# Kernel optimization log

Measured on AMD Instinct MI355X. Metric: run time of the kernel, lower is better.

## Reference

```python
import jax, jax.numpy as jnp
import numpy as np

D_MODEL = 256
NHEAD = 8
D_HEAD = D_MODEL // NHEAD
DIM_FF = 1024
B, L = 4, 16384
LN_EPS = 1e-5


def _layernorm(x, g, b):
    mu = jnp.mean(x, axis=-1, keepdims=True)
    var = jnp.mean((x - mu) ** 2, axis=-1, keepdims=True)
    return (x - mu) * jax.lax.rsqrt(var + LN_EPS) * g + b


def _phi(x):
    # elu(x) + 1
    return jnp.where(x > 0, x + 1.0, jnp.exp(x))


def setup_inputs() -> dict:
    key = jax.random.key(0)
    ks = jax.random.split(key, 16)
    s_in = 1.0 / np.sqrt(D_MODEL)
    s_ff = 1.0 / np.sqrt(DIM_FF)
    inp = {
        "x": jax.random.normal(ks[0], (B, L, D_MODEL), dtype=jnp.float32),
        "Wq": jax.random.normal(ks[1], (D_MODEL, D_MODEL), dtype=jnp.float32) * s_in,
        "bq": jnp.zeros((D_MODEL,), jnp.float32),
        "Wk": jax.random.normal(ks[2], (D_MODEL, D_MODEL), dtype=jnp.float32) * s_in,
        "bk": jnp.zeros((D_MODEL,), jnp.float32),
        "Wv": jax.random.normal(ks[3], (D_MODEL, D_MODEL), dtype=jnp.float32) * s_in,
        "bv": jnp.zeros((D_MODEL,), jnp.float32),
        "Wo": jax.random.normal(ks[4], (D_MODEL, D_MODEL), dtype=jnp.float32) * s_in,
        "bo": jnp.zeros((D_MODEL,), jnp.float32),
        "W1": jax.random.normal(ks[5], (D_MODEL, DIM_FF), dtype=jnp.float32) * s_in,
        "b1": jnp.zeros((DIM_FF,), jnp.float32),
        "W2": jax.random.normal(ks[6], (DIM_FF, D_MODEL), dtype=jnp.float32) * s_ff,
        "b2": jnp.zeros((D_MODEL,), jnp.float32),
        "ln1_g": jnp.ones((D_MODEL,), jnp.float32),
        "ln1_b": jnp.zeros((D_MODEL,), jnp.float32),
        "ln2_g": jnp.ones((D_MODEL,), jnp.float32),
        "ln2_b": jnp.zeros((D_MODEL,), jnp.float32),
    }
    return inp


def reference(x, Wq, bq, Wk, bk, Wv, bv, Wo, bo, W1, b1, W2, b2, ln1_g, ln1_b, ln2_g, ln2_b):
    Bq, Lq, _ = x.shape
    q = (x @ Wq + bq).reshape(Bq, Lq, NHEAD, D_HEAD)
    k = (x @ Wk + bk).reshape(Bq, Lq, NHEAD, D_HEAD)
    v = (x @ Wv + bv).reshape(Bq, Lq, NHEAD, D_HEAD)
    q_phi = _phi(q)
    k_phi = _phi(k)
    # kv: [B, H, d, e]
    kv = jnp.einsum("blhd,blhe->bhde", k_phi, v)
    k_sum = k_phi.sum(axis=1)  # [B, H, d]
    z = 1.0 / (jnp.einsum("blhd,bhd->blh", q_phi, k_sum) + 1e-6)
    out = jnp.einsum("blhd,bhde,blh->blhe", q_phi, kv, z)
    out = out.reshape(Bq, Lq, D_MODEL) @ Wo + bo
    x = _layernorm(x + out, ln1_g, ln1_b)
    ff = jax.nn.relu(x @ W1 + b1) @ W2 + b2
    x = _layernorm(x + ff, ln2_g, ln2_b)
    return x
```

## Files before the change

kernel.cpp:

```cpp
#include <hip/hip_runtime.h>
#include <hip/hip_bf16.h>
#include <math.h>

#define NTOK   65536
#define L_SEQ  16384

typedef __bf16 bf16_t;
typedef bf16_t bf16x8 __attribute__((ext_vector_type(8)));
typedef bf16_t bf16x4 __attribute__((ext_vector_type(4)));
typedef float  f32x4  __attribute__((ext_vector_type(4)));

__device__ inline float phi_f(float x) { return x > 0.f ? x + 1.f : __expf(x); }

__device__ inline float quad_sum(float v) {
    v += __shfl_xor(v, 1);
    v += __shfl_xor(v, 2);
    v += __shfl_xor(v, 4);
    v += __shfl_xor(v, 8);
    return v;
}

__device__ inline float ld_any(const void* p, size_t i, int f32) {
    return f32 ? ((const float*)p)[i] : (float)((const bf16_t*)p)[i];
}

__device__ inline void async_copy16(const bf16_t* g, bf16_t* l) {
    __builtin_amdgcn_global_load_lds(
        (const __attribute__((address_space(1))) unsigned int*)g,
        (__attribute__((address_space(3))) unsigned int*)l, 16, 0, 0);
}

__device__ inline void stage_swz(const bf16_t* __restrict__ g, bf16_t* lds,
                                 int tid, int nslot, int ulog2, int rowstride) {
    const int umask = (1 << ulog2) - 1;
    for (int s = tid; s < nslot; s += 256) {
        int n = s >> ulog2, j = s & umask;
        int u = j ^ (n & umask);
        async_copy16(g + (size_t)n * rowstride + u * 8, lds + (size_t)s * 8);
    }
}

__device__ inline bf16x8 rd_swz(const bf16_t* lds, int n, int u, int ulog2) {
    int j = u ^ (n & ((1 << ulog2) - 1));
    return *(const bf16x8*)&lds[(((size_t)n << ulog2) + j) * 8];
}

__device__ inline void stage_w2ff(const bf16_t* __restrict__ W2_t, int ch,
                                  bf16_t* lds, int tid) {
    for (int S = tid; S < 1024; S += 256) {
        int r = S >> 3, phys = S & 7;
        int u = phys ^ (r & 7);
        int n = ((u >> 2) << 7) + r;
        int ks = u & 3;
        async_copy16(W2_t + (size_t)n * 1024 + ch * 32 + ks * 8, lds + (size_t)S * 8);
    }
}

__device__ inline bf16x8 rd_w2ff(const bf16_t* lds, int n, int quad) {
    int r = n & 127;
    int u = ((n >> 7) << 2) + quad;
    int phys = u ^ (r & 7);
    return *(const bf16x8*)&lds[(size_t)(r * 8 + phys) * 8];
}

__device__ inline void hs_put(bf16_t* hs, int r, int c, bf16_t v) {
    int phys = (c >> 3) ^ (r & 15);
    hs[r * 128 + phys * 8 + (c & 7)] = v;
}
__device__ inline bf16x8 hs_get8(const bf16_t* hs, int r, int u) {
    int phys = u ^ (r & 15);
    return *(const bf16x8*)&hs[r * 128 + phys * 8];
}

__device__ inline void ld_afrags(const bf16_t* __restrict__ tile, int row, int q8,
                                 bf16x8 a[8]) {
#pragma unroll
    for (int kk = 0; kk < 8; ++kk)
        a[kk] = *(const bf16x8*)&tile[(size_t)row * 256 + kk * 32 + q8];
}

__global__ __launch_bounds__(256) void k_detect(const void* __restrict__ xraw,
                                                int* __restrict__ flag) {
    __shared__ int bad;
    if (threadIdx.x == 0) bad = 0;
    __syncthreads();
    const bf16_t* xb = (const bf16_t*)xraw;
    int mybad = 0;
#pragma unroll
    for (int j = 0; j < 16; ++j) {
        float v = fabsf((float)xb[threadIdx.x + 256 * j]);
        if (!(v <= 1000.f)) mybad = 1;
    }
    if (mybad) atomicOr(&bad, 1);
    __syncthreads();
    if (threadIdx.x == 0) *flag = bad;
}

__global__ __launch_bounds__(256) void k_convert(const void* __restrict__ xraw,
                                                 const int* __restrict__ flag,
                                                 bf16_t* __restrict__ xbf) {
    const int f = *flag;
    size_t i = ((size_t)blockIdx.x * 256 + threadIdx.x) * 4;
    if (f) {
        f32x4 v = *(const f32x4*)((const float*)xraw + i);
        bf16x4 o;
#pragma unroll
        for (int j = 0; j < 4; ++j) o[j] = (bf16_t)v[j];
        *(bf16x4*)&xbf[i] = o;
    } else {
        *(bf16x4*)&xbf[i] = *(const bf16x4*)((const bf16_t*)xraw + i);
    }
}

__global__ __launch_bounds__(256) void k_prep(
    const void* __restrict__ Wq, const void* __restrict__ Wk,
    const void* __restrict__ Wv, const void* __restrict__ Wo,
    const void* __restrict__ W1, const void* __restrict__ W2,
    const void* __restrict__ bq, const void* __restrict__ bk,
    const void* __restrict__ bv, const void* __restrict__ bo,
    const void* __restrict__ b1, const void* __restrict__ b2,
    const void* __restrict__ g1, const void* __restrict__ be1,
    const void* __restrict__ g2, const void* __restrict__ be2,
    const int* __restrict__ flag,
    bf16_t* __restrict__ Wqkv_t, bf16_t* __restrict__ Wo_t,
    bf16_t* __restrict__ W1_t, bf16_t* __restrict__ W2_t,
    bf16_t* __restrict__ pbuf, float* __restrict__ kvbuf) {
    const int f = *flag;
    int idx = blockIdx.x * 256 + threadIdx.x;
    if (idx < 196608) {
        int n = idx >> 8, k = idx & 255;
        float v;
        if (n < 256)      v = ld_any(Wq, k * 256 + n, f);
        else if (n < 512) v = ld_any(Wk, k * 256 + (n - 256), f);
        else              v = ld_any(Wv, k * 256 + (n - 512), f);
        Wqkv_t[idx] = (bf16_t)v;
    } else if (idx < 262144) {
        int i = idx - 196608; int n = i >> 8, k = i & 255;
        Wo_t[i] = (bf16_t)ld_any(Wo, k * 256 + n, f);
    } else if (idx < 524288) {
        int i = idx - 262144; int n = i >> 8, k = i & 255;
        W1_t[i] = (bf16_t)ld_any(W1, k * 1024 + n, f);
    } else if (idx < 786432) {
        int i = idx - 524288; int n = i >> 10, k = i & 1023;
        W2_t[i] = (bf16_t)ld_any(W2, k * 256 + n, f);
    } else if (idx < 820224) {
        kvbuf[idx - 786432] = 0.f;
    } else if (idx < 823552) {
        int i = idx - 820224;
        float v;
        if (i < 256)        v = ld_any(bq, i, f);
        else if (i < 512)   v = ld_any(bk, i - 256, f);
        else if (i < 768)   v = ld_any(bv, i - 512, f);
        else if (i < 1024)  v = ld_any(bo, i - 768, f);
        else if (i < 2048)  v = ld_any(b1, i - 1024, f);
        else if (i < 2304)  v = ld_any(b2, i - 2048, f);
        else if (i < 2560)  v = ld_any(g1, i - 2304, f);
        else if (i < 2816)  v = ld_any(be1, i - 2560, f);
        else if (i < 3072)  v = ld_any(g2, i - 2816, f);
        else                v = ld_any(be2, i - 3072, f);
        pbuf[i] = (bf16_t)v;
    }
}

__global__ __launch_bounds__(256, 3) void k_qkv(
    const bf16_t* __restrict__ x, const bf16_t* __restrict__ Wqkv_t,
    const bf16_t* __restrict__ pbuf, bf16_t* __restrict__ q_phi) {
    const int mt = blockIdx.x, nt = blockIdx.y;
    const int tid = threadIdx.x, wave = tid >> 6, lane = tid & 63;
    const int l15 = lane & 15, quad = lane >> 4, q8 = quad * 8;
    __shared__ __align__(16) bf16_t bs[128 * 256];
    const int m0 = mt * 128;
    bf16x8 a[2][8];
    ld_afrags(x + (size_t)m0 * 256,        wave * 16 + l15, q8, a[0]);
    ld_afrags(x + (size_t)(m0 + 64) * 256, wave * 16 + l15, q8, a[1]);
    stage_swz(Wqkv_t + (size_t)nt * 128 * 256, bs, tid, 4096, 5, 256);
    __syncthreads();
    f32x4 acc[2][8] = {};
#pragma unroll
    for (int kk = 0; kk < 8; ++kk) {
#pragma unroll
        for (int s = 0; s < 8; ++s) {
            bf16x8 b = rd_swz(bs, s * 16 + l15, kk * 4 + quad, 5);
            acc[0][s] = __builtin_amdgcn_mfma_f32_16x16x32_bf16(a[0][kk], b, acc[0][s], 0, 0, 0);
            acc[1][s] = __builtin_amdgcn_mfma_f32_16x16x32_bf16(a[1][kk], b, acc[1][s], 0, 0, 0);
        }
    }
#pragma unroll
    for (int s = 0; s < 8; ++s) {
        int ng = nt * 128 + s * 16 + l15;
        float bias = (float)pbuf[ng];
#pragma unroll
        for (int mm = 0; mm < 2; ++mm) {
#pragma unroll
            for (int r = 0; r < 4; ++r) {
                int m = m0 + mm * 64 + wave * 16 + quad * 4 + r;
                q_phi[(size_t)m * 256 + ng] = (bf16_t)phi_f(acc[mm][s][r] + bias);
            }
        }
    }
}

__global__ __launch_bounds__(256, 4) void k_kv(
    const bf16_t* __restrict__ x, const bf16_t* __restrict__ Wqkv_t,
    const bf16_t* __restrict__ pbuf, float* __restrict__ kvbuf) {
    const int mt = blockIdx.x, hg = blockIdx.y;
    const int tid = threadIdx.x, wave = tid >> 6, lane = tid & 63;
    const int l15 = lane & 15, quad = lane >> 4, q8 = quad * 8;
    __shared__ __align__(16) bf16_t stg[8192];
    __shared__ __align__(16) bf16_t hsK[4096];
    __shared__ __align__(16) bf16_t hsV[4096];
    const int m0 = mt * 128;
    const int b = m0 >> 14;
    bf16x8 a[2][8];
    ld_afrags(x + (size_t)m0 * 256,        wave * 16 + l15, q8, a[0]);
    ld_afrags(x + (size_t)(m0 + 64) * 256, wave * 16 + l15, q8, a[1]);
    const int td = wave >> 1, te = wave & 1;
    for (int h4 = 0; h4 < 4; ++h4) {
        const int head = hg * 4 + h4;
        const size_t kvbase = (size_t)(b * 8 + head) * 1056;
        stage_swz(Wqkv_t + (size_t)(256 + head * 32) * 256, stg, tid, 1024, 5, 256);
        __syncthreads();
        {
            f32x4 acck[2][2] = {};
#pragma unroll
            for (int kk = 0; kk < 8; ++kk) {
#pragma unroll
                for (int s = 0; s < 2; ++s) {
                    bf16x8 bb = rd_swz(stg, s * 16 + l15, kk * 4 + quad, 5);
                    acck[0][s] = __builtin_amdgcn_mfma_f32_16x16x32_bf16(a[0][kk], bb, acck[0][s], 0, 0, 0);
                    acck[1][s] = __builtin_amdgcn_mfma_f32_16x16x32_bf16(a[1][kk], bb, acck[1][s], 0, 0, 0);
                }
            }
#pragma unroll
            for (int s = 0; s < 2; ++s) {
                float bias = (float)pbuf[256 + head * 32 + s * 16 + l15];
                float kst = 0.f;
#pragma unroll
                for (int mm = 0; mm < 2; ++mm) {
#pragma unroll
                    for (int r = 0; r < 4; ++r) {
                        float v = phi_f(acck[mm][s][r] + bias);
                        kst += v;
                        int c = mm * 64 + wave * 16 + quad * 4 + r;
                        hs_put(hsK, s * 16 + l15, c, (bf16_t)v);
                    }
                }
                kst += __shfl_xor(kst, 16);
                kst += __shfl_xor(kst, 32);
                if (quad == 0)
                    atomicAdd(&kvbuf[kvbase + 1024 + s * 16 + l15], kst);
            }
        }
        __syncthreads();
        stage_swz(Wqkv_t + (size_t)(512 + head * 32) * 256, stg, tid, 1024, 5, 256);
        __syncthreads();
        {
            f32x4 accv[2][2] = {};
#pragma unroll
            for (int kk = 0; kk < 8; ++kk) {
#pragma unroll
                for (int s = 0; s < 2; ++s) {
                    bf16x8 bb = rd_swz(stg, s * 16 + l15, kk * 4 + quad, 5);
                    accv[0][s] = __builtin_amdgcn_mfma_f32_16x16x32_bf16(a[0][kk], bb, accv[0][s], 0, 0, 0);
                    accv[1][s] = __builtin_amdgcn_mfma_f32_16x16x32_bf16(a[1][kk], bb, accv[1][s], 0, 0, 0);
                }
            }
#pragma unroll
            for (int s = 0; s < 2; ++s) {
                float bias = (float)pbuf[512 + head * 32 + s * 16 + l15];
#pragma unroll
                for (int mm = 0; mm < 2; ++mm) {
#pragma unroll
                    for (int r = 0; r < 4; ++r) {
                        int c = mm * 64 + wave * 16 + quad * 4 + r;
                        hs_put(hsV, s * 16 + l15, c, (bf16_t)(accv[mm][s][r] + bias));
                    }
                }
            }
        }
        __syncthreads();
        {
            f32x4 kvacc = {};
#pragma unroll
            for (int kk = 0; kk < 4; ++kk) {
                bf16x8 ak = hs_get8(hsK, td * 16 + l15, kk * 4 + quad);
                bf16x8 bv = hs_get8(hsV, te * 16 + l15, kk * 4 + quad);
                kvacc = __builtin_amdgcn_mfma_f32_16x16x32_bf16(ak, bv, kvacc, 0, 0, 0);
            }
#pragma unroll
            for (int r = 0; r < 4; ++r) {
                int d = td * 16 + quad * 4 + r;
                int e = te * 16 + l15;
                atomicAdd(&kvbuf[kvbase + e * 32 + d], kvacc[r]);
            }
        }
    }
}

__global__ __launch_bounds__(256) void k_kvprep(const float* __restrict__ kvbuf,
                                                bf16_t* __restrict__ kvbf) {
    int idx = blockIdx.x * 256 + threadIdx.x;
    int bh = idx >> 8, r4 = (idx & 255) * 4;
    f32x4 v = *(const f32x4*)&kvbuf[(size_t)bh * 1056 + r4];
    bf16x4 o;
#pragma unroll
    for (int j = 0; j < 4; ++j) o[j] = (bf16_t)v[j];
    *(bf16x4*)&kvbf[(size_t)bh * 1024 + r4] = o;
}

__global__ __launch_bounds__(256, 2) void k_attn_wo_ln1(
    const bf16_t* __restrict__ q_phi, const bf16_t* __restrict__ kvbf,
    const float* __restrict__ kvbuf, const bf16_t* __restrict__ Wo_t,
    const bf16_t* __restrict__ pbuf, const void* __restrict__ xraw,
    const int* __restrict__ flag, bf16_t* __restrict__ x1) {
    const int f = *flag;
    const int mt = blockIdx.x;
    const int tid = threadIdx.x, wave = tid >> 6, lane = tid & 63;
    const int l15 = lane & 15, quad = lane >> 4, q8 = quad * 8;
    __shared__ __align__(16) bf16_t sm0[8192];
    __shared__ __align__(16) bf16_t sm1[16896];
    const int m0 = mt * 128;
    const int b = m0 >> 14;
    stage_swz(Wo_t, sm0, tid, 1024, 5, 256);
    bf16_t* hs = sm1 + wave * (16 * 264);
    const bf16_t* kvb = kvbf + (size_t)b * 8192;
    const float*  ksb = kvbuf + (size_t)b * 8448;
    bf16x8 a2[2][8];
#pragma unroll
    for (int mm = 0; mm < 2; ++mm) {
        bf16x8 a[8];
        ld_afrags(q_phi + (size_t)(m0 + mm * 64) * 256, wave * 16 + l15, q8, a);
#pragma unroll
        for (int h = 0; h < 8; ++h) {
            f32x4 ks0 = *(const f32x4*)&ksb[h * 1056 + 1024 + q8];
            f32x4 ks1 = *(const f32x4*)&ksb[h * 1056 + 1024 + q8 + 4];
            float den = 0.f;
#pragma unroll
            for (int j = 0; j < 4; ++j) den += (float)a[h][j] * ks0[j];
#pragma unroll
            for (int j = 0; j < 4; ++j) den += (float)a[h][4 + j] * ks1[j];
            den += __shfl_xor(den, 16);
            den += __shfl_xor(den, 32);
            float z = 1.f / (den + 1e-6f);
            float zr[4];
#pragma unroll
            for (int r = 0; r < 4; ++r) zr[r] = __shfl(z, quad * 4 + r, 16);
            bf16x8 b0 = *(const bf16x8*)&kvb[h * 1024 + l15 * 32 + q8];
            bf16x8 b1 = *(const bf16x8*)&kvb[h * 1024 + (16 + l15) * 32 + q8];
            f32x4 at0 = {}, at1 = {};
            at0 = __builtin_amdgcn_mfma_f32_16x16x32_bf16(a[h], b0, at0, 0, 0, 0);
            at1 = __builtin_amdgcn_mfma_f32_16x16x32_bf16(a[h], b1, at1, 0, 0, 0);
#pragma unroll
            for (int r = 0; r < 4; ++r) {
                hs[(quad * 4 + r) * 264 + h * 32 + l15]      = (bf16_t)(at0[r] * zr[r]);
                hs[(quad * 4 + r) * 264 + h * 32 + 16 + l15] = (bf16_t)(at1[r] * zr[r]);
            }
        }
#pragma unroll
        for (int kk = 0; kk < 8; ++kk)
            a2[mm][kk] = *(const bf16x8*)&hs[l15 * 264 + kk * 32 + q8];
    }
    __syncthreads();
    f32x4 acc[2][16] = {};
    for (int nc = 0; nc < 8; ++nc) {
        if (nc < 7) stage_swz(Wo_t + (size_t)(nc + 1) * 32 * 256,
                              (nc & 1) ? sm0 : sm1, tid, 1024, 5, 256);
        const bf16_t* buf = (nc & 1) ? sm1 : sm0;
#pragma unroll
        for (int kk = 0; kk < 8; ++kk) {
#pragma unroll
            for (int s = 0; s < 2; ++s) {
                bf16x8 bb = rd_swz(buf, s * 16 + l15, kk * 4 + quad, 5);
                acc[0][nc * 2 + s] = __builtin_amdgcn_mfma_f32_16x16x32_bf16(a2[0][kk], bb, acc[0][nc * 2 + s], 0, 0, 0);
                acc[1][nc * 2 + s] = __builtin_amdgcn_mfma_f32_16x16x32_bf16(a2[1][kk], bb, acc[1][nc * 2 + s], 0, 0, 0);
            }
        }
        __syncthreads();
    }
#pragma unroll
    for (int mm = 0; mm < 2; ++mm) {
        float s1[4] = {}, s2[4] = {};
#pragma unroll
        for (int s = 0; s < 16; ++s) {
            int n = s * 16 + l15;
            float bias = (float)pbuf[768 + n];
#pragma unroll
            for (int r = 0; r < 4; ++r) {
                int m = m0 + mm * 64 + wave * 16 + quad * 4 + r;
                float val = acc[mm][s][r] + bias + ld_any(xraw, (size_t)m * 256 + n, f);
                acc[mm][s][r] = val;
                s1[r] += val; s2[r] += val * val;
            }
        }
#pragma unroll
        for (int r = 0; r < 4; ++r) {
            float ts = quad_sum(s1[r]), ts2 = quad_sum(s2[r]);
            float mu = ts * (1.f / 256.f);
            float rs = rsqrtf(ts2 * (1.f / 256.f) - mu * mu + 1e-5f);
            s1[r] = mu; s2[r] = rs;
        }
#pragma unroll
        for (int s = 0; s < 16; ++s) {
            int n = s * 16 + l15;
            float gn = (float)pbuf[2304 + n], bn = (float)pbuf[2560 + n];
#pragma unroll
            for (int r = 0; r < 4; ++r) {
                int m = m0 + mm * 64 + wave * 16 + quad * 4 + r;
                x1[(size_t)m * 256 + n] = (bf16_t)((acc[mm][s][r] - s1[r]) * s2[r] * gn + bn);
            }
        }
    }
}

__global__ __launch_bounds__(256, 2) void k_ff_ln2(
    const bf16_t* __restrict__ x1, const bf16_t* __restrict__ W1_t,
    const bf16_t* __restrict__ W2_t, const bf16_t* __restrict__ pbuf,
    const int* __restrict__ flag, void* __restrict__ out) {
    const int f32o = *flag;
    const int mt = blockIdx.x;
    const int tid = threadIdx.x, wave = tid >> 6, lane = tid & 63;
    const int l15 = lane & 15, quad = lane >> 4, q8 = quad * 8;
    __shared__ __align__(16) bf16_t w1s[2][8192];
    __shared__ __align__(16) bf16_t w2s[2][8192];
    __shared__ __align__(16) bf16_t hs[4][2][16][40];
    const int m0 = mt * 128 + wave * 32;
    bf16x8 a[2][8];
    ld_afrags(x1 + (size_t)m0 * 256, l15,      q8, a[0]);
    ld_afrags(x1 + (size_t)m0 * 256, 16 + l15, q8, a[1]);
    stage_swz(W1_t, w1s[0], tid, 1024, 5, 256);
    stage_w2ff(W2_t, 0, w2s[0], tid);
    __syncthreads();
    f32x4 acc[2][16] = {};
    for (int ch = 0; ch < 32; ++ch) {
        const int cur = ch & 1;
        if (ch < 31) {
            stage_swz(W1_t + (size_t)(ch + 1) * 32 * 256, w1s[cur ^ 1], tid, 1024, 5, 256);
            stage_w2ff(W2_t, ch + 1, w2s[cur ^ 1], tid);
        }
        f32x4 h0[2] = {}, h1[2] = {};
#pragma unroll
        for (int kk = 0; kk < 8; ++kk) {
#pragma unroll
            for (int s = 0; s < 2; ++s) {
                bf16x8 b = rd_swz(w1s[cur], s * 16 + l15, kk * 4 + quad, 5);
                h0[s] = __builtin_amdgcn_mfma_f32_16x16x32_bf16(a[0][kk], b, h0[s], 0, 0, 0);
                h1[s] = __builtin_amdgcn_mfma_f32_16x16x32_bf16(a[1][kk], b, h1[s], 0, 0, 0);
            }
        }
#pragma unroll
        for (int s = 0; s < 2; ++s) {
            float bias = (float)pbuf[1024 + ch * 32 + s * 16 + l15];
#pragma unroll
            for (int r = 0; r < 4; ++r) {
                float v0 = h0[s][r] + bias;
                float v1 = h1[s][r] + bias;
                hs[wave][0][quad * 4 + r][s * 16 + l15] = (bf16_t)(v0 > 0.f ? v0 : 0.f);
                hs[wave][1][quad * 4 + r][s * 16 + l15] = (bf16_t)(v1 > 0.f ? v1 : 0.f);
            }
        }
        bf16x8 a2_0 = *(const bf16x8*)&hs[wave][0][l15][q8];
        bf16x8 a2_1 = *(const bf16x8*)&hs[wave][1][l15][q8];
#pragma unroll
        for (int s = 0; s < 16; ++s) {
            bf16x8 b0 = rd_w2ff(w2s[cur], s * 16 + l15, quad);
            acc[0][s] = __builtin_amdgcn_mfma_f32_16x16x32_bf16(a2_0, b0, acc[0][s], 0, 0, 0);
            acc[1][s] = __builtin_amdgcn_mfma_f32_16x16x32_bf16(a2_1, b0, acc[1][s], 0, 0, 0);
        }
        __syncthreads();
    }
#pragma unroll
    for (int mm = 0; mm < 2; ++mm) {
        float s1[4] = {}, s2[4] = {};
#pragma unroll
        for (int s = 0; s < 16; ++s) {
            int n = s * 16 + l15;
            float bias = (float)pbuf[2048 + n];
#pragma unroll
            for (int r = 0; r < 4; ++r) {
                int m = m0 + mm * 16 + quad * 4 + r;
                float val = acc[mm][s][r] + bias + (float)x1[(size_t)m * 256 + n];
                acc[mm][s][r] = val;
                s1[r] += val; s2[r] += val * val;
            }
        }
#pragma unroll
        for (int r = 0; r < 4; ++r) {
            float ts = quad_sum(s1[r]), ts2 = quad_sum(s2[r]);
            float mu = ts * (1.f / 256.f);
            float rs = rsqrtf(ts2 * (1.f / 256.f) - mu * mu + 1e-5f);
            s1[r] = mu; s2[r] = rs;
        }
#pragma unroll
        for (int s = 0; s < 16; ++s) {
            int n = s * 16 + l15;
            float gn = (float)pbuf[2816 + n], bn = (float)pbuf[3072 + n];
#pragma unroll
            for (int r = 0; r < 4; ++r) {
                int m = m0 + mm * 16 + quad * 4 + r;
                float val = (acc[mm][s][r] - s1[r]) * s2[r] * gn + bn;
                if (f32o) ((float*)out)[(size_t)m * 256 + n] = val;
                else      ((bf16_t*)out)[(size_t)m * 256 + n] = (bf16_t)val;
            }
        }
    }
}

extern "C" void kernel_launch(void* const* d_in, const int* in_sizes, int n_in,
                              void* d_out, int out_size, void* d_ws, size_t ws_size,
                              hipStream_t stream) {
    char* ws = (char*)d_ws;
    int*    flag   = (int*)ws;
    bf16_t* xbf    = (bf16_t*)(ws + 256);
    bf16_t* Wqkv_t = (bf16_t*)(ws + 33554688);
    bf16_t* Wo_t   = (bf16_t*)(ws + 33947904);
    bf16_t* W1_t   = (bf16_t*)(ws + 34078976);
    bf16_t* W2_t   = (bf16_t*)(ws + 34603264);
    bf16_t* pbuf   = (bf16_t*)(ws + 35127552);
    float*  kvbuf  = (float*)(ws + 35134208);
    bf16_t* bufQ   = (bf16_t*)(ws + 35269376);
    bf16_t* kvbf   = bufQ + (size_t)NTOK * 256;
    bf16_t* bufX1  = bufQ;

    k_detect<<<1, 256, 0, stream>>>(d_in[0], flag);
    k_convert<<<16384, 256, 0, stream>>>(d_in[0], flag, xbf);
    k_prep<<<3217, 256, 0, stream>>>(d_in[1], d_in[3], d_in[5], d_in[7],
                                     d_in[9], d_in[11],
                                     d_in[2], d_in[4], d_in[6], d_in[8],
                                     d_in[10], d_in[12],
                                     d_in[13], d_in[14], d_in[15], d_in[16],
                                     flag, Wqkv_t, Wo_t, W1_t, W2_t, pbuf, kvbuf);
    k_qkv<<<dim3(512, 2), 256, 0, stream>>>(xbf, Wqkv_t, pbuf, bufQ);
    k_kv<<<dim3(512, 2), 256, 0, stream>>>(xbf, Wqkv_t, pbuf, kvbuf);
    k_kvprep<<<32, 256, 0, stream>>>(kvbuf, kvbf);
    k_attn_wo_ln1<<<512, 256, 0, stream>>>(bufQ, kvbf, kvbuf, Wo_t, pbuf,
                                           d_in[0], flag, bufX1);
    k_ff_ln2<<<512, 256, 0, stream>>>(bufX1, W1_t, W2_t, pbuf, flag, d_out);
}
```

Measured before the change: 440.2 us.

## Replace global atomic KV accumulation with per-tile partials and a reduction kernel

The k_kv kernel now writes each token tile's KV outer-product and k_sum partials to a dedicated slice of a partial buffer instead of atomically adding into a shared accumulator. The per-wave k_sum values are combined in shared memory first. A new k_kvred kernel sums the 128 partial slices per (batch, head), writes the float result, and also produces the bf16 copy, replacing k_kvprep. This removes heavy atomic contention on the same 1056 floats per head. In exchange it adds a workspace buffer of about 17 MB plus an extra read pass over it.

```diff
diff --git a/kernel.cpp b/kernel.cpp
--- a/kernel.cpp
+++ b/kernel.cpp
@@ -202,13 +202,14 @@
 
 __global__ __launch_bounds__(256, 4) void k_kv(
     const bf16_t* __restrict__ x, const bf16_t* __restrict__ Wqkv_t,
-    const bf16_t* __restrict__ pbuf, float* __restrict__ kvbuf) {
+    const bf16_t* __restrict__ pbuf, float* __restrict__ kvpart) {
     const int mt = blockIdx.x, hg = blockIdx.y;
     const int tid = threadIdx.x, wave = tid >> 6, lane = tid & 63;
     const int l15 = lane & 15, quad = lane >> 4, q8 = quad * 8;
     __shared__ __align__(16) bf16_t stg[8192];
     __shared__ __align__(16) bf16_t hsK[4096];
     __shared__ __align__(16) bf16_t hsV[4096];
+    __shared__ float ksred[4][32];
     const int m0 = mt * 128;
     const int b = m0 >> 14;
     bf16x8 a[2][8];
@@ -217,7 +218,7 @@
     const int td = wave >> 1, te = wave & 1;
     for (int h4 = 0; h4 < 4; ++h4) {
         const int head = hg * 4 + h4;
-        const size_t kvbase = (size_t)(b * 8 + head) * 1056;
+        float* dst = kvpart + ((size_t)(b * 8 + head) * 128 + (mt & 127)) * 1056;
         stage_swz(Wqkv_t + (size_t)(256 + head * 32) * 256, stg, tid, 1024, 5, 256);
         __syncthreads();
         {
@@ -247,8 +248,7 @@
                 }
                 kst += __shfl_xor(kst, 16);
                 kst += __shfl_xor(kst, 32);
-                if (quad == 0)
-                    atomicAdd(&kvbuf[kvbase + 1024 + s * 16 + l15], kst);
+                if (quad == 0) ksred[wave][s * 16 + l15] = kst;
             }
         }
         __syncthreads();
@@ -287,25 +287,26 @@
                 bf16x8 bv = hs_get8(hsV, te * 16 + l15, kk * 4 + quad);
                 kvacc = __builtin_amdgcn_mfma_f32_16x16x32_bf16(ak, bv, kvacc, 0, 0, 0);
             }
-#pragma unroll
-            for (int r = 0; r < 4; ++r) {
-                int d = td * 16 + quad * 4 + r;
-                int e = te * 16 + l15;
-                atomicAdd(&kvbuf[kvbase + e * 32 + d], kvacc[r]);
-            }
-        }
-    }
-}
-
-__global__ __launch_bounds__(256) void k_kvprep(const float* __restrict__ kvbuf,
-                                                bf16_t* __restrict__ kvbf) {
-    int idx = blockIdx.x * 256 + threadIdx.x;
-    int bh = idx >> 8, r4 = (idx & 255) * 4;
-    f32x4 v = *(const f32x4*)&kvbuf[(size_t)bh * 1056 + r4];
-    bf16x4 o;
-#pragma unroll
-    for (int j = 0; j < 4; ++j) o[j] = (bf16_t)v[j];
-    *(bf16x4*)&kvbf[(size_t)bh * 1024 + r4] = o;
+            int e = te * 16 + l15;
+            *(f32x4*)&dst[e * 32 + td * 16 + quad * 4] = kvacc;
+        }
+        if (tid < 32)
+            dst[1024 + tid] = ksred[0][tid] + ksred[1][tid] + ksred[2][tid] + ksred[3][tid];
+    }
+}
+
+__global__ __launch_bounds__(256) void k_kvred(const float* __restrict__ kvpart,
+                                               float* __restrict__ kvbuf,
+                                               bf16_t* __restrict__ kvbf) {
+    const int bh = blockIdx.x;
+    const int idx = blockIdx.y * 256 + threadIdx.x;
+    if (idx >= 1056) return;
+    const float* p = kvpart + (size_t)bh * 128 * 1056 + idx;
+    float s = 0.f;
+#pragma unroll 4
+    for (int sl = 0; sl < 128; ++sl) s += p[(size_t)sl * 1056];
+    kvbuf[(size_t)bh * 1056 + idx] = s;
+    if (idx < 1024) kvbf[(size_t)bh * 1024 + idx] = (bf16_t)s;
 }
 
 __global__ __launch_bounds__(256, 2) void k_attn_wo_ln1(
@@ -519,6 +520,7 @@
     float*  kvbuf  = (float*)(ws + 35134208);
     bf16_t* bufQ   = (bf16_t*)(ws + 35269376);
     bf16_t* kvbf   = bufQ + (size_t)NTOK * 256;
+    float*  kvpart = (float*)(ws + 35269376 + 2u * NTOK * 256 + 65536);
     bf16_t* bufX1  = bufQ;
 
     k_detect<<<1, 256, 0, stream>>>(d_in[0], flag);
@@ -530,8 +532,8 @@
                                      d_in[13], d_in[14], d_in[15], d_in[16],
                                      flag, Wqkv_t, Wo_t, W1_t, W2_t, pbuf, kvbuf);
     k_qkv<<<dim3(512, 2), 256, 0, stream>>>(xbf, Wqkv_t, pbuf, bufQ);
-    k_kv<<<dim3(512, 2), 256, 0, stream>>>(xbf, Wqkv_t, pbuf, kvbuf);
-    k_kvprep<<<32, 256, 0, stream>>>(kvbuf, kvbf);
+    k_kv<<<dim3(512, 2), 256, 0, stream>>>(xbf, Wqkv_t, pbuf, kvpart);
+    k_kvred<<<dim3(32, 5), 256, 0, stream>>>(kvpart, kvbuf, kvbf);
     k_attn_wo_ln1<<<512, 256, 0, stream>>>(bufQ, kvbf, kvbuf, Wo_t, pbuf,
                                            d_in[0], flag, bufX1);
     k_ff_ln2<<<512, 256, 0, stream>>>(bufX1, W1_t, W2_t, pbuf, flag, d_out);
```

After: 364.6 us. 1.21x faster.
